# Kernel optimization log

Measured on AMD Instinct MI355X. Metric: run time of the kernel, lower is better.

The kernel has to match this reference:

```python
import jax, jax.numpy as jnp
import numpy as np

B, S, C = 16, 2048, 512
E = S            # embed_dim == seq_len (RMSNorm applied on transposed seq axis)
H = 4 * E        # FFN hidden
LAMBDA_INIT = float(0.8 - 0.6 * np.exp(-0.3 * 1.0))  # layer_index = 1
SCALE = E ** (-0.25)
K = 5            # decomposition moving-average kernel


def rmsnorm(x, w, eps=1e-8):
    return x * jax.lax.rsqrt(jnp.mean(x * x, axis=-1, keepdims=True) + eps) * w


def decompose(a):
    # DLinear-style series decomposition: replicate-padded moving average along seq
    pad = (K - 1) // 2
    ap = jnp.concatenate([jnp.repeat(a[:, :1], pad, axis=1), a, jnp.repeat(a[:, -1:], pad, axis=1)], axis=1)
    n = a.shape[1]
    trend = sum(ap[:, i:i + n] for i in range(K)) / K
    return trend, a - trend


def setup_inputs() -> dict:
    key = jax.random.key(0)
    ks = jax.random.split(key, 12)
    p = lambda i, shape, s=0.02: jax.random.normal(ks[i], shape, jnp.float32) * s
    return {
        "x": jax.random.normal(ks[0], (B, S, C), jnp.float32),
        "ln_attn_w": jnp.ones((E,), jnp.float32),
        "q12_w": p(1, (E, 2 * E)), "q12_b": jnp.zeros((2 * E,), jnp.float32),
        "k12_w": p(2, (E, 2 * E)), "k12_b": jnp.zeros((2 * E,), jnp.float32),
        "v_w": p(3, (E, E)), "v_b": jnp.zeros((E,), jnp.float32),
        "lambda_q1": p(4, (E,), 0.1), "lambda_k1": p(5, (E,), 0.1),
        "lambda_q2": p(6, (E,), 0.1), "lambda_k2": p(7, (E,), 0.1),
        "norm_w": jnp.ones((E,), jnp.float32),
        "ln_ff_w": jnp.ones((E,), jnp.float32),
        "ff_w1": p(8, (E, H)), "ff_b1": jnp.zeros((H,), jnp.float32),
        "ff_w2": p(9, (H, E)), "ff_b2": jnp.zeros((E,), jnp.float32),
    }


def reference(x, ln_attn_w, q12_w, q12_b, k12_w, k12_b, v_w, v_b,
              lambda_q1, lambda_k1, lambda_q2, lambda_k2,
              norm_w, ln_ff_w, ff_w1, ff_b1, ff_w2, ff_b2):
    # pre-attention RMSNorm over the seq axis (via transpose)
    a = jnp.swapaxes(rmsnorm(jnp.swapaxes(x, -1, -2), ln_attn_w), -1, -2)  # [B,S,C]
    trend, seasonal = decompose(a)
    # project seq dim of trend/seasonal (iTransformer style: channels are tokens)
    q = jnp.swapaxes(trend, -1, -2) @ q12_w + q12_b      # [B,C,2S]
    q1, q2 = jnp.split(q, 2, axis=-1)                    # [B,C,S] each
    k = jnp.swapaxes(seasonal, -1, -2) @ k12_w + k12_b   # [B,C,2S]
    k1, k2 = jnp.split(k, 2, axis=-1)                    # [B,C,S]
    v = jnp.swapaxes(a, -1, -2) @ v_w + v_b              # [B,C,S]
    a1 = jnp.einsum('bis,bjs->bij', q1, k1) * SCALE      # [B,C,C]
    a2 = jnp.einsum('bis,bjs->bij', q2, k2) * SCALE      # [B,C,C]
    lam = jnp.exp(jnp.sum(lambda_q1 * lambda_k1)) - jnp.exp(jnp.sum(lambda_q2 * lambda_k2)) + LAMBDA_INIT
    d = jax.nn.softmax(a1, axis=-1) - lam * jax.nn.softmax(a2, axis=-1)
    attn = rmsnorm(d @ v, norm_w) * (1.0 - LAMBDA_INIT)  # [B,C,S]
    x = x + jnp.swapaxes(attn, -1, -2)
    # FFN over the seq axis
    h = rmsnorm(jnp.swapaxes(x, -1, -2), ln_ff_w)        # [B,C,S]
    ff = jax.nn.gelu(h @ ff_w1 + ff_b1, approximate=False) @ ff_w2 + ff_b2
    return x + jnp.swapaxes(ff, -1, -2)
```

## Files before the change

kernel.cpp:

```cpp
#include <hip/hip_runtime.h>
#include <hip/hip_bf16.h>

#define B_ 16
#define S_ 2048
#define C_ 512
#define H_ 8192

#define LAMBDA_INIT_F 0.3555090675909693f
#define ONE_M_LI_F    0.6444909324090307f
#define SCALE_F       0.14865088937534013f

using bf16x8 = __attribute__((ext_vector_type(8))) short;
using f32x4  = __attribute__((ext_vector_type(4))) float;

__device__ __forceinline__ float b2f(ushort u) {
  union { unsigned u; float f; } x; x.u = ((unsigned)u) << 16; return x.f;
}
__device__ __forceinline__ ushort f2b(float f) {
  union { float f; unsigned u; } x; x.f = f;
  unsigned r = x.u + 0x7fffu + ((x.u >> 16) & 1u);
  return (ushort)(r >> 16);
}

__device__ __forceinline__ void load_lds16(const void* g, void* s) {
  __builtin_amdgcn_global_load_lds((const __attribute__((address_space(1))) void*)g,
                                   (__attribute__((address_space(3))) void*)s,
                                   16, 0, 0);
}

#define WAITV4() do { asm volatile("s_waitcnt vmcnt(4)" ::: "memory"); __builtin_amdgcn_sched_barrier(0); } while (0)
#define WAITV0() do { asm volatile("s_waitcnt vmcnt(0)" ::: "memory"); __builtin_amdgcn_sched_barrier(0); } while (0)
#define WAITL0() do { asm volatile("s_waitcnt lgkmcnt(0)" ::: "memory"); __builtin_amdgcn_sched_barrier(0); } while (0)
#define BAR()    __builtin_amdgcn_s_barrier()

template <int EPI>
__global__ __launch_bounds__(512, 1) void gemm256(
    const ushort* __restrict__ A, const ushort* __restrict__ Bt,
    ushort* __restrict__ C, const float* __restrict__ bias,
    const ushort* __restrict__ addm,
    int K, int lda, int ldb, int ldc)
{
  __shared__ ushort lds[65536];
  const int t = threadIdx.x, w = t >> 6, lane = t & 63;
  const int fr = lane & 15, khl = lane >> 4;
  const int wr = w >> 2, wc = w & 3;

  const int gx = gridDim.x;
  const int id = blockIdx.y * gx + blockIdx.x;
  const int nwg = gx * gridDim.y;
  const int swz = (id & 7) * (nwg >> 3) + (id >> 3);
  const int m0 = (swz % gx) * 256, n0 = (swz / gx) * 256;

  const int sl    = (t & 7) ^ ((t >> 3) & 7);
  const int rbase = ((t >> 3) << 1) + (sl >> 2);
  const int khs   = sl & 3;
  const size_t aoff = (size_t)(m0 + rbase) * lda + khs * 8;
  const size_t boff = (size_t)(n0 + rbase) * ldb + khs * 8;
  const size_t jstA = (size_t)128 * lda, jstB = (size_t)128 * ldb;

  int ao[8], bo[4];
#pragma unroll
  for (int m = 0; m < 8; ++m) {
    const int row = wr * 128 + m * 16 + fr, dr = row >> 1;
    const int so = (((row & 1) << 2) + khl) ^ (dr & 7);
    ao[m] = dr * 64 + so * 8;
  }
#pragma unroll
  for (int n = 0; n < 4; ++n) {
    const int row = wc * 64 + n * 16 + fr, dr = row >> 1;
    const int so = (((row & 1) << 2) + khl) ^ (dr & 7);
    bo[n] = 16384 + dr * 64 + so * 8;
  }

  f32x4 acc[8][4] = {};
  const int NT = K >> 6;

#define STAGE_A(ch, nb, k1) do { const ushort* s_ = A + aoff + (k1) + (ch) * 32; \
    ushort* d_ = &lds[(nb) + (ch) * 8192 + w * 512]; \
    load_lds16(s_, d_); load_lds16(s_ + jstA, d_ + 4096); } while (0)
#define STAGE_B(ch, nb, k1) do { const ushort* s_ = Bt + boff + (k1) + (ch) * 32; \
    ushort* d_ = &lds[(nb) + 16384 + (ch) * 8192 + w * 512]; \
    load_lds16(s_, d_); load_lds16(s_ + jstB, d_ + 4096); } while (0)
#define LDA(cb, ch, m) (*(const bf16x8*)&lds[(cb) + (ch) * 8192 + ao[m]])
#define LDB(cb, ch, n) (*(const bf16x8*)&lds[(cb) + (ch) * 8192 + bo[n]])
#define MFMA8(mlo, nf, bg) _Pragma("unroll") for (int m_ = 0; m_ < 8; ++m_) \
    acc[m_][nf] = __builtin_amdgcn_mfma_f32_16x16x32_bf16(af[m_], bg, acc[m_][nf], 0, 0, 0)

  STAGE_A(0, 0, 0); STAGE_B(0, 0, 0); STAGE_A(1, 0, 0); STAGE_B(1, 0, 0);
  WAITV4(); BAR();

  bf16x8 af[8];
  for (int kt = 0; kt < NT - 1; ++kt) {
    const int cb = (kt & 1) << 15, nb = cb ^ 32768;
    const int k1 = (kt + 1) << 6;
    bf16x8 b0, b1;
#pragma unroll
    for (int m = 0; m < 8; ++m) af[m] = LDA(cb, 0, m);
    b0 = LDB(cb, 0, 0); b1 = LDB(cb, 0, 1);
    STAGE_A(0, nb, k1);
    BAR(); WAITL0();
    __builtin_amdgcn_s_setprio(1); MFMA8(0, 0, b0); MFMA8(0, 1, b1); __builtin_amdgcn_s_setprio(0);
    BAR();
    b0 = LDB(cb, 0, 2); b1 = LDB(cb, 0, 3);
    STAGE_B(0, nb, k1);
    WAITV4(); BAR(); WAITL0();
    __builtin_amdgcn_s_setprio(1); MFMA8(0, 2, b0); MFMA8(0, 3, b1); __builtin_amdgcn_s_setprio(0);
    BAR();
#pragma unroll
    for (int m = 0; m < 8; ++m) af[m] = LDA(cb, 1, m);
    b0 = LDB(cb, 1, 0); b1 = LDB(cb, 1, 1);
    STAGE_A(1, nb, k1);
    BAR(); WAITL0();
    __builtin_amdgcn_s_setprio(1); MFMA8(1, 0, b0); MFMA8(1, 1, b1); __builtin_amdgcn_s_setprio(0);
    BAR();
    b0 = LDB(cb, 1, 2); b1 = LDB(cb, 1, 3);
    STAGE_B(1, nb, k1);
    WAITV4(); BAR(); WAITL0();
    __builtin_amdgcn_s_setprio(1); MFMA8(1, 2, b0); MFMA8(1, 3, b1); __builtin_amdgcn_s_setprio(0);
    BAR();
  }
  {
    const int cb = ((NT - 1) & 1) << 15;
    bf16x8 b0, b1;
#pragma unroll
    for (int m = 0; m < 8; ++m) af[m] = LDA(cb, 0, m);
    b0 = LDB(cb, 0, 0); b1 = LDB(cb, 0, 1);
    BAR(); WAITL0();
    MFMA8(0, 0, b0); MFMA8(0, 1, b1);
    BAR();
    b0 = LDB(cb, 0, 2); b1 = LDB(cb, 0, 3);
    WAITV0(); BAR(); WAITL0();
    MFMA8(0, 2, b0); MFMA8(0, 3, b1);
    BAR();
#pragma unroll
    for (int m = 0; m < 8; ++m) af[m] = LDA(cb, 1, m);
    b0 = LDB(cb, 1, 0); b1 = LDB(cb, 1, 1);
    BAR(); WAITL0();
    MFMA8(1, 0, b0); MFMA8(1, 1, b1);
    BAR();
    b0 = LDB(cb, 1, 2); b1 = LDB(cb, 1, 3);
    BAR(); WAITL0();
    MFMA8(1, 2, b0); MFMA8(1, 3, b1);
  }
#undef STAGE_A
#undef STAGE_B
#undef LDA
#undef LDB
#undef MFMA8

  const int r0 = khl * 4;
#pragma unroll
  for (int m = 0; m < 8; ++m)
#pragma unroll
    for (int nf = 0; nf < 4; ++nf) {
      const int gr = m0 + wr * 128 + m * 16 + r0;
      const int gc = n0 + wc * 64 + nf * 16 + fr;
      const float bb = (EPI == 3) ? 0.f : bias[gc];
#pragma unroll
      for (int r = 0; r < 4; ++r) {
        const size_t idx = (size_t)(gr + r) * ldc + gc;
        float v = acc[m][nf][r];
        if constexpr (EPI == 1) v += bb;
        if constexpr (EPI == 2) { v += bb; v = 0.5f * v * (1.f + erff(v * 0.7071067811865475f)); }
        if constexpr (EPI == 4) v += bb + b2f(addm[idx]) + b2f(C[idx]);
        C[idx] = f2b(v);
      }
    }
}

template <int EPI>
__global__ __launch_bounds__(256, 2) void gemm_nt(
    const ushort* __restrict__ Aall, const ushort* __restrict__ Ball,
    void* __restrict__ Call, int K, int lda, int ldb, int ldc,
    long sA, long sB, long sC, long sA2, long sB2, float alpha)
{
  __shared__ ushort lA[4096];
  __shared__ ushort lB[4096];
  const int t = threadIdx.x;
  const int m0 = blockIdx.x * 128, n0 = blockIdx.y * 128;
  const int zb = blockIdx.z & 15, zh = blockIdx.z >> 4;
  const ushort* A  = Aall + (size_t)zb * sA + (size_t)zh * sA2;
  const ushort* Bt = Ball + (size_t)zb * sB + (size_t)zh * sB2;
  const int lane = t & 63;
  const int wave = t >> 6;
  const int wm = (wave >> 1) * 64, wn = (wave & 1) * 64;
  const int fr = lane & 15, kh = lane >> 4;
  f32x4 acc[4][4] = {};
  const int srow = t >> 2;
  const int scol = (t & 3) * 8;
  const size_t ar0 = (size_t)(m0 + srow) * lda + scol;
  const size_t ar1 = (size_t)(m0 + 64 + srow) * lda + scol;
  const size_t br0 = (size_t)(n0 + srow) * ldb + scol;
  const size_t br1 = (size_t)(n0 + 64 + srow) * ldb + scol;
  const int wbase = wave * 512;

  for (int k0 = 0; k0 < K; k0 += 32) {
    __syncthreads();
    load_lds16(A + ar0 + k0,  &lA[wbase]);
    load_lds16(A + ar1 + k0,  &lA[2048 + wbase]);
    load_lds16(Bt + br0 + k0, &lB[wbase]);
    load_lds16(Bt + br1 + k0, &lB[2048 + wbase]);
    __syncthreads();
    bf16x8 af[4], bg[4];
#pragma unroll
    for (int i = 0; i < 4; ++i)
      af[i] = *(const bf16x8*)&lA[(wm + i * 16 + fr) * 32 + kh * 8];
#pragma unroll
    for (int j = 0; j < 4; ++j)
      bg[j] = *(const bf16x8*)&lB[(wn + j * 16 + fr) * 32 + kh * 8];
#pragma unroll
    for (int i = 0; i < 4; ++i)
#pragma unroll
      for (int j = 0; j < 4; ++j)
        acc[i][j] = __builtin_amdgcn_mfma_f32_16x16x32_bf16(af[i], bg[j], acc[i][j], 0, 0, 0);
  }

  const int r0 = kh * 4;
  if constexpr (EPI == 0) {
    float* C = (float*)Call + (size_t)blockIdx.z * sC;
#pragma unroll
    for (int i = 0; i < 4; ++i)
#pragma unroll
      for (int j = 0; j < 4; ++j) {
        const int gr = m0 + wm + i * 16 + r0;
        const int gc = n0 + wn + j * 16 + fr;
#pragma unroll
        for (int r = 0; r < 4; ++r)
          C[(size_t)(gr + r) * ldc + gc] = acc[i][j][r] * alpha;
      }
  } else {
    ushort* C = (ushort*)Call + (size_t)blockIdx.z * sC;
#pragma unroll
    for (int i = 0; i < 4; ++i)
#pragma unroll
      for (int j = 0; j < 4; ++j) {
        const int gr = m0 + wm + i * 16 + r0;
        const int gc = n0 + wn + j * 16 + fr;
#pragma unroll
        for (int r = 0; r < 4; ++r)
          C[(size_t)(gr + r) * ldc + gc] = f2b(acc[i][j][r] * alpha);
      }
  }
}

__device__ __forceinline__ float block_sum(float v, float* red) {
#pragma unroll
  for (int o = 32; o > 0; o >>= 1) v += __shfl_down(v, o, 64);
  __syncthreads();
  if ((threadIdx.x & 63) == 0) red[threadIdx.x >> 6] = v;
  __syncthreads();
  return red[0] + red[1] + red[2] + red[3];
}
__device__ __forceinline__ float block_max(float v, float* red) {
#pragma unroll
  for (int o = 32; o > 0; o >>= 1) v = fmaxf(v, __shfl_down(v, o, 64));
  __syncthreads();
  if ((threadIdx.x & 63) == 0) red[threadIdx.x >> 6] = v;
  __syncthreads();
  return fmaxf(fmaxf(red[0], red[1]), fmaxf(red[2], red[3]));
}

__global__ __launch_bounds__(256) void k_rms_part(const float* __restrict__ x, float* __restrict__ part) {
  const int c = blockIdx.x * 256 + threadIdx.x;
  const int sl = blockIdx.y;
  const int b = blockIdx.z;
  const float* p = x + (size_t)b * S_ * C_ + c;
  const int s0 = sl * 256;
  float s = 0.f;
  for (int i = 0; i < 256; ++i) { float v = p[(size_t)(s0 + i) * C_]; s += v * v; }
  part[((size_t)b * C_ + c) * 8 + sl] = s;
}
__global__ __launch_bounds__(256) void k_rms_fin(const float* __restrict__ part, float* __restrict__ rms1) {
  const int i = blockIdx.x * 256 + threadIdx.x;
  const float* p = part + (size_t)i * 8;
  float s = 0.f;
#pragma unroll
  for (int j = 0; j < 8; ++j) s += p[j];
  rms1[i] = rsqrtf(s * (1.f / S_) + 1e-8f);
}

__global__ __launch_bounds__(256) void k_trans_norm(const float* __restrict__ x, const float* __restrict__ rms1,
                                                    const float* __restrict__ w,
                                                    ushort* __restrict__ aT, ushort* __restrict__ xT) {
  __shared__ float tile[32][33];
  const int s0 = blockIdx.x * 32, c0 = blockIdx.y * 32, b = blockIdx.z;
  const int tx = threadIdx.x, ty = threadIdx.y;
  const float* xb = x + (size_t)b * S_ * C_;
#pragma unroll
  for (int r = 0; r < 4; ++r) {
    const int s = ty + 8 * r;
    tile[s][tx] = xb[(size_t)(s0 + s) * C_ + c0 + tx];
  }
  __syncthreads();
#pragma unroll
  for (int r = 0; r < 4; ++r) {
    const int c = ty + 8 * r;
    const float v = tile[tx][c];
    const float rm = rms1[b * C_ + c0 + c];
    const size_t o = ((size_t)b * C_ + c0 + c) * S_ + s0 + tx;
    xT[o] = f2b(v);
    aT[o] = f2b(v * rm * w[s0 + tx]);
  }
}

__global__ __launch_bounds__(256) void k_wtrans(const float* __restrict__ W, ushort* __restrict__ WT,
                                                int Kd, int Ndstride, int n_base) {
  __shared__ float tile[32][33];
  const int k0 = blockIdx.x * 32, n0 = blockIdx.y * 32;
  const int tx = threadIdx.x, ty = threadIdx.y;
#pragma unroll
  for (int r = 0; r < 4; ++r) {
    const int k = ty + 8 * r;
    tile[k][tx] = W[(size_t)(k0 + k) * Ndstride + n_base + n0 + tx];
  }
  __syncthreads();
#pragma unroll
  for (int r = 0; r < 4; ++r) {
    const int n = ty + 8 * r;
    WT[(size_t)(n0 + n) * Kd + k0 + tx] = f2b(tile[tx][n]);
  }
}

__global__ __launch_bounds__(256) void k_bt(const ushort* __restrict__ in, ushort* __restrict__ out, int R, int CL) {
  __shared__ ushort tile[32][33];
  const int r0 = blockIdx.x * 32, c0 = blockIdx.y * 32;
  const size_t zb = (size_t)blockIdx.z * R * CL;
  const int tx = threadIdx.x, ty = threadIdx.y;
#pragma unroll
  for (int r = 0; r < 4; ++r) {
    const int rr = ty + 8 * r;
    tile[rr][tx] = in[zb + (size_t)(r0 + rr) * CL + c0 + tx];
  }
  __syncthreads();
#pragma unroll
  for (int r = 0; r < 4; ++r) {
    const int cc = ty + 8 * r;
    out[zb + (size_t)(c0 + cc) * R + r0 + tx] = tile[tx][cc];
  }
}

__device__ __forceinline__ float trend5(const ushort* p, int s) {
  float sum = 0.f;
#pragma unroll
  for (int d = -2; d <= 2; ++d) {
    int ss = s + d; ss = ss < 0 ? 0 : (ss > S_ - 1 ? S_ - 1 : ss);
    sum += b2f(p[ss]);
  }
  return sum * 0.2f;
}
__global__ __launch_bounds__(256) void k_dtrend(const ushort* __restrict__ aT, ushort* __restrict__ trT) {
  const size_t i = (size_t)blockIdx.x * 256 + threadIdx.x;
  const int s = (int)(i & (S_ - 1));
  trT[i] = f2b(trend5(aT + (i - s), s));
}
__global__ __launch_bounds__(256) void k_dseason(const ushort* __restrict__ aT, ushort* __restrict__ seT) {
  const size_t i = (size_t)blockIdx.x * 256 + threadIdx.x;
  const int s = (int)(i & (S_ - 1));
  const ushort* p = aT + (i - s);
  seT[i] = f2b(b2f(p[s]) - trend5(p, s));
}

__global__ __launch_bounds__(256) void k_lambda(const float* __restrict__ lq1, const float* __restrict__ lk1,
                                                const float* __restrict__ lq2, const float* __restrict__ lk2,
                                                float* __restrict__ lam) {
  __shared__ float r1[4], r2[4];
  const int t = threadIdx.x;
  float s1 = 0.f, s2 = 0.f;
  for (int i = t; i < S_; i += 256) { s1 += lq1[i] * lk1[i]; s2 += lq2[i] * lk2[i]; }
#pragma unroll
  for (int o = 32; o > 0; o >>= 1) { s1 += __shfl_down(s1, o, 64); s2 += __shfl_down(s2, o, 64); }
  if ((t & 63) == 0) { r1[t >> 6] = s1; r2[t >> 6] = s2; }
  __syncthreads();
  if (t == 0) {
    const float a = r1[0] + r1[1] + r1[2] + r1[3];
    const float b = r2[0] + r2[1] + r2[2] + r2[3];
    *lam = expf(a) - expf(b) + LAMBDA_INIT_F;
  }
}

__global__ __launch_bounds__(256) void k_softmax(const float* __restrict__ a1, const float* __restrict__ a2,
                                                 const float* __restrict__ lamp, ushort* __restrict__ dm) {
  __shared__ float red[4];
  const size_t row = blockIdx.x;
  const float* p1 = a1 + row * 512;
  const float* p2 = a2 + row * 512;
  const int t = threadIdx.x;
  const float v1a = p1[t], v1b = p1[t + 256];
  const float v2a = p2[t], v2b = p2[t + 256];
  const float m1 = block_max(fmaxf(v1a, v1b), red);
  const float m2 = block_max(fmaxf(v2a, v2b), red);
  const float e1a = expf(v1a - m1), e1b = expf(v1b - m1);
  const float e2a = expf(v2a - m2), e2b = expf(v2b - m2);
  const float s1 = block_sum(e1a + e1b, red);
  const float s2 = block_sum(e2a + e2b, red);
  const float i1 = 1.f / s1, i2 = (*lamp) / s2;
  ushort* o = dm + row * 512;
  o[t]       = f2b(e1a * i1 - e2a * i2);
  o[t + 256] = f2b(e1b * i1 - e2b * i2);
}

__global__ __launch_bounds__(256) void k_postattn(const ushort* __restrict__ P, const ushort* __restrict__ xT,
                                                  const float* __restrict__ norm_w, const float* __restrict__ ln_ff_w,
                                                  ushort* __restrict__ attn, ushort* __restrict__ h) {
  __shared__ float red[4];
  const size_t row = blockIdx.x;
  const ushort* p = P + row * S_;
  const int t = threadIdx.x;
  float v[8]; float ss = 0.f;
#pragma unroll
  for (int i = 0; i < 8; ++i) { v[i] = b2f(p[t + 256 * i]); ss += v[i] * v[i]; }
  ss = block_sum(ss, red);
  const float inv = rsqrtf(ss * (1.f / S_) + 1e-8f);
  const ushort* xr = xT + row * S_;
  ushort* ar = attn + row * S_;
  float x2[8]; float ss2 = 0.f;
#pragma unroll
  for (int i = 0; i < 8; ++i) {
    const int s = t + 256 * i;
    const float at = v[i] * inv * norm_w[s] * ONE_M_LI_F;
    ar[s] = f2b(at);
    const float xx = b2f(xr[s]) + at;
    x2[i] = xx; ss2 += xx * xx;
  }
  ss2 = block_sum(ss2, red);
  const float inv2 = rsqrtf(ss2 * (1.f / S_) + 1e-8f);
  ushort* hr = h + row * S_;
#pragma unroll
  for (int i = 0; i < 8; ++i) { const int s = t + 256 * i; hr[s] = f2b(x2[i] * inv2 * ln_ff_w[s]); }
}

__global__ __launch_bounds__(256) void k_final2(const float* __restrict__ x, const ushort* __restrict__ sumT,
                                                float* __restrict__ out) {
  __shared__ float tile[32][33];
  const int s0 = blockIdx.x * 32, c0 = blockIdx.y * 32, b = blockIdx.z;
  const int tx = threadIdx.x, ty = threadIdx.y;
#pragma unroll
  for (int r = 0; r < 4; ++r) {
    const int c = ty + 8 * r;
    tile[c][tx] = b2f(sumT[((size_t)b * C_ + c0 + c) * S_ + s0 + tx]);
  }
  __syncthreads();
#pragma unroll
  for (int r = 0; r < 4; ++r) {
    const int s = ty + 8 * r;
    const size_t o = ((size_t)b * S_ + s0 + s) * C_ + c0 + tx;
    out[o] = x[o] + tile[tx][s];
  }
}

__global__ void k_probe(float* out, float v) { out[0] = v; }

extern "C" void kernel_launch(void* const* d_in, const int* in_sizes, int n_in,
                              void* d_out, int out_size, void* d_ws, size_t ws_size,
                              hipStream_t stream) {
  const float* x       = (const float*)d_in[0];
  const float* ln_attn = (const float*)d_in[1];
  const float* q12_w   = (const float*)d_in[2];
  const float* q12_b   = (const float*)d_in[3];
  const float* k12_w   = (const float*)d_in[4];
  const float* k12_b   = (const float*)d_in[5];
  const float* v_w     = (const float*)d_in[6];
  const float* v_b     = (const float*)d_in[7];
  const float* lq1     = (const float*)d_in[8];
  const float* lk1     = (const float*)d_in[9];
  const float* lq2     = (const float*)d_in[10];
  const float* lk2     = (const float*)d_in[11];
  const float* norm_w  = (const float*)d_in[12];
  const float* ln_ff   = (const float*)d_in[13];
  const float* ff_w1   = (const float*)d_in[14];
  const float* ff_b1   = (const float*)d_in[15];
  const float* ff_w2   = (const float*)d_in[16];
  const float* ff_b2   = (const float*)d_in[17];
  float* out = (float*)d_out;

  if (ws_size < 184844544ull) {
    k_probe<<<1, 1, 0, stream>>>(out, (float)(ws_size >> 20));
    return;
  }

  char* ws = (char*)d_ws;
  ushort* slotA = (ushort*)(ws + 0);
  ushort* slotB = (ushort*)(ws + 33554432);
  ushort* slotC = (ushort*)(ws + 67108864);
  ushort* slotD = (ushort*)(ws + 100663296);
  ushort* slotE = (ushort*)(ws + 134217728);
  ushort* slotF = (ushort*)(ws + 167772160);
  float*  part  = (float*) (ws + 184549376);
  float*  rms1  = (float*) (ws + 184811520);
  float*  lamp  = (float*) (ws + 184844288);

  ushort* aT   = slotA;
  ushort* xT   = slotE;
  ushort* Vm   = slotB;
  ushort* VT   = slotD;
  ushort* trT  = slotB;
  ushort* seT  = slotC;
  ushort* K12  = slotA;
  float*  scr  = (float*)slotC;
  ushort* Pm   = slotB;
  ushort* attn = slotC;
  ushort* hbuf = slotA;
  ushort* ff1T = slotB;
  ushort* ff2T = slotD;
  ushort* ffo  = slotE;
  ushort* wsl  = slotF;
  ushort* dmat = slotF;
  ushort* Qm   = (ushort*)d_out;
  ushort* H1   = (ushort*)d_out;

  const dim3 blk256(256), blk512(512), blkT(32, 8);

  k_rms_part<<<dim3(2, 8, B_), blk256, 0, stream>>>(x, part);
  k_rms_fin<<<dim3(32), blk256, 0, stream>>>(part, rms1);
  k_trans_norm<<<dim3(64, 16, B_), blkT, 0, stream>>>(x, rms1, ln_attn, aT, xT);

  k_wtrans<<<dim3(64, 64), blkT, 0, stream>>>(v_w, wsl, 2048, 2048, 0);
  gemm256<1><<<dim3(32, 8), blk512, 0, stream>>>(aT, wsl, Vm, v_b, nullptr, 2048, 2048, 2048, 2048);
  k_bt<<<dim3(16, 64, B_), blkT, 0, stream>>>(Vm, VT, 512, 2048);

  k_dtrend<<<dim3(65536), blk256, 0, stream>>>(aT, trT);
  k_wtrans<<<dim3(64, 128), blkT, 0, stream>>>(q12_w, wsl, 2048, 4096, 0);
  gemm256<1><<<dim3(32, 16), blk512, 0, stream>>>(trT, wsl, Qm, q12_b, nullptr, 2048, 2048, 2048, 4096);

  k_dseason<<<dim3(65536), blk256, 0, stream>>>(aT, seT);
  k_lambda<<<dim3(1), blk256, 0, stream>>>(lq1, lk1, lq2, lk2, lamp);
  k_wtrans<<<dim3(64, 128), blkT, 0, stream>>>(k12_w, wsl, 2048, 4096, 0);
  gemm256<1><<<dim3(32, 16), blk512, 0, stream>>>(seT, wsl, K12, k12_b, nullptr, 2048, 2048, 2048, 4096);

  gemm_nt<0><<<dim3(4, 4, 32), blk256, 0, stream>>>(Qm, K12, scr, 2048, 4096, 4096, 512,
                                                    512L * 4096, 512L * 4096, 512L * 512,
                                                    2048L, 2048L, SCALE_F);

  k_softmax<<<dim3(8192), blk256, 0, stream>>>(scr, scr + 4194304, lamp, dmat);
  gemm_nt<3><<<dim3(4, 16, B_), blk256, 0, stream>>>(dmat, VT, Pm, 512, 512, 512, 2048,
                                                     512L * 512, 2048L * 512, 512L * 2048,
                                                     0, 0, 1.f);

  k_postattn<<<dim3(8192), blk256, 0, stream>>>(Pm, xT, norm_w, ln_ff, attn, hbuf);

  k_wtrans<<<dim3(64, 256), blkT, 0, stream>>>(ff_w1, ff1T, 2048, 8192, 0);
  k_wtrans<<<dim3(256, 64), blkT, 0, stream>>>(ff_w2, ff2T, 8192, 2048, 0);

  gemm256<2><<<dim3(32, 16), blk512, 0, stream>>>(hbuf, ff1T, H1, ff_b1, nullptr,
                                                  2048, 2048, 2048, 4096);
  gemm256<3><<<dim3(32, 8), blk512, 0, stream>>>(H1, ff2T, ffo, nullptr, nullptr,
                                                 4096, 4096, 8192, 2048);
  gemm256<2><<<dim3(32, 16), blk512, 0, stream>>>(hbuf, ff1T + (size_t)4096 * 2048, H1,
                                                  ff_b1 + 4096, nullptr, 2048, 2048, 2048, 4096);
  gemm256<4><<<dim3(32, 8), blk512, 0, stream>>>(H1, ff2T + 4096, ffo, ff_b2, attn,
                                                 4096, 4096, 8192, 2048);

  k_final2<<<dim3(64, 16, B_), blkT, 0, stream>>>(x, ffo, out);
}
```

Before: 1.329 ms.

## Restructure GEMM LDS pipeline into four 32-wide K stages with deeper prefetch

Measured after the change: 1.346 ms. No clear change (+1.3%).

```diff
diff --git a/kernel.cpp b/kernel.cpp
--- a/kernel.cpp
+++ b/kernel.cpp
@@ -28,6 +28,7 @@
                                    16, 0, 0);
 }
 
+#define WAITV8() do { asm volatile("s_waitcnt vmcnt(8)" ::: "memory"); __builtin_amdgcn_sched_barrier(0); } while (0)
 #define WAITV4() do { asm volatile("s_waitcnt vmcnt(4)" ::: "memory"); __builtin_amdgcn_sched_barrier(0); } while (0)
 #define WAITV0() do { asm volatile("s_waitcnt vmcnt(0)" ::: "memory"); __builtin_amdgcn_sched_barrier(0); } while (0)
 #define WAITL0() do { asm volatile("s_waitcnt lgkmcnt(0)" ::: "memory"); __builtin_amdgcn_sched_barrier(0); } while (0)
@@ -51,101 +52,111 @@
   const int swz = (id & 7) * (nwg >> 3) + (id >> 3);
   const int m0 = (swz % gx) * 256, n0 = (swz / gx) * 256;
 
-  const int sl    = (t & 7) ^ ((t >> 3) & 7);
-  const int rbase = ((t >> 3) << 1) + (sl >> 2);
-  const int khs   = sl & 3;
-  const size_t aoff = (size_t)(m0 + rbase) * lda + khs * 8;
-  const size_t boff = (size_t)(n0 + rbase) * ldb + khs * 8;
+  const int rs = t >> 2;
+  const int cs = (t & 3) ^ (rs & 3);
+  const size_t aoff = (size_t)(m0 + rs) * lda + cs * 8;
+  const size_t boff = (size_t)(n0 + rs) * ldb + cs * 8;
   const size_t jstA = (size_t)128 * lda, jstB = (size_t)128 * ldb;
 
   int ao[8], bo[4];
 #pragma unroll
   for (int m = 0; m < 8; ++m) {
-    const int row = wr * 128 + m * 16 + fr, dr = row >> 1;
-    const int so = (((row & 1) << 2) + khl) ^ (dr & 7);
-    ao[m] = dr * 64 + so * 8;
+    const int row = wr * 128 + m * 16 + fr;
+    ao[m] = row * 32 + ((khl ^ (row & 3)) * 8);
   }
 #pragma unroll
   for (int n = 0; n < 4; ++n) {
-    const int row = wc * 64 + n * 16 + fr, dr = row >> 1;
-    const int so = (((row & 1) << 2) + khl) ^ (dr & 7);
-    bo[n] = 16384 + dr * 64 + so * 8;
+    const int row = wc * 64 + n * 16 + fr;
+    bo[n] = 8192 + row * 32 + ((khl ^ (row & 3)) * 8);
   }
 
   f32x4 acc[8][4] = {};
   const int NT = K >> 6;
 
-#define STAGE_A(ch, nb, k1) do { const ushort* s_ = A + aoff + (k1) + (ch) * 32; \
-    ushort* d_ = &lds[(nb) + (ch) * 8192 + w * 512]; \
+#define STAGE_A(u) do { const ushort* s_ = A + aoff + (size_t)(u) * 32; \
+    ushort* d_ = &lds[((u) & 3) * 16384 + w * 512]; \
     load_lds16(s_, d_); load_lds16(s_ + jstA, d_ + 4096); } while (0)
-#define STAGE_B(ch, nb, k1) do { const ushort* s_ = Bt + boff + (k1) + (ch) * 32; \
-    ushort* d_ = &lds[(nb) + 16384 + (ch) * 8192 + w * 512]; \
+#define STAGE_B(u) do { const ushort* s_ = Bt + boff + (size_t)(u) * 32; \
+    ushort* d_ = &lds[((u) & 3) * 16384 + 8192 + w * 512]; \
     load_lds16(s_, d_); load_lds16(s_ + jstB, d_ + 4096); } while (0)
-#define LDA(cb, ch, m) (*(const bf16x8*)&lds[(cb) + (ch) * 8192 + ao[m]])
-#define LDB(cb, ch, n) (*(const bf16x8*)&lds[(cb) + (ch) * 8192 + bo[n]])
-#define MFMA8(mlo, nf, bg) _Pragma("unroll") for (int m_ = 0; m_ < 8; ++m_) \
+#define LDA8(u) _Pragma("unroll") for (int m_ = 0; m_ < 8; ++m_) \
+    af[m_] = *(const bf16x8*)&lds[((u) & 3) * 16384 + ao[m_]]
+#define LDB1(u, n) (*(const bf16x8*)&lds[((u) & 3) * 16384 + bo[n]])
+#define MFMA8(nf, bg) _Pragma("unroll") for (int m_ = 0; m_ < 8; ++m_) \
     acc[m_][nf] = __builtin_amdgcn_mfma_f32_16x16x32_bf16(af[m_], bg, acc[m_][nf], 0, 0, 0)
-
-  STAGE_A(0, 0, 0); STAGE_B(0, 0, 0); STAGE_A(1, 0, 0); STAGE_B(1, 0, 0);
-  WAITV4(); BAR();
-
-  bf16x8 af[8];
-  for (int kt = 0; kt < NT - 1; ++kt) {
-    const int cb = (kt & 1) << 15, nb = cb ^ 32768;
-    const int k1 = (kt + 1) << 6;
-    bf16x8 b0, b1;
-#pragma unroll
-    for (int m = 0; m < 8; ++m) af[m] = LDA(cb, 0, m);
-    b0 = LDB(cb, 0, 0); b1 = LDB(cb, 0, 1);
-    STAGE_A(0, nb, k1);
-    BAR(); WAITL0();
-    __builtin_amdgcn_s_setprio(1); MFMA8(0, 0, b0); MFMA8(0, 1, b1); __builtin_amdgcn_s_setprio(0);
+#define PRIO1() __builtin_amdgcn_s_setprio(1)
+#define PRIO0() __builtin_amdgcn_s_setprio(0)
+
+  STAGE_A(0); STAGE_B(0); STAGE_A(1); STAGE_B(1); STAGE_A(2); STAGE_B(2);
+  WAITV8(); BAR();
+
+  bf16x8 af[8], b0, b1;
+  for (int kt = 0; kt < NT - 2; ++kt) {
+    const int u0 = 2 * kt, u1 = u0 + 1;
+    LDA8(u0); b0 = LDB1(u0, 0); b1 = LDB1(u0, 1);
+    STAGE_A(u0 + 3);
+    BAR(); WAITL0();
+    PRIO1(); MFMA8(0, b0); MFMA8(1, b1); PRIO0();
     BAR();
-    b0 = LDB(cb, 0, 2); b1 = LDB(cb, 0, 3);
-    STAGE_B(0, nb, k1);
-    WAITV4(); BAR(); WAITL0();
-    __builtin_amdgcn_s_setprio(1); MFMA8(0, 2, b0); MFMA8(0, 3, b1); __builtin_amdgcn_s_setprio(0);
+    b0 = LDB1(u0, 2); b1 = LDB1(u0, 3);
+    STAGE_B(u0 + 3);
+    BAR(); WAITL0();
+    PRIO1(); MFMA8(2, b0); MFMA8(3, b1); PRIO0();
+    WAITV8(); BAR();
+    LDA8(u1); b0 = LDB1(u1, 0); b1 = LDB1(u1, 1);
+    STAGE_A(u0 + 4);
+    BAR(); WAITL0();
+    PRIO1(); MFMA8(0, b0); MFMA8(1, b1); PRIO0();
     BAR();
-#pragma unroll
-    for (int m = 0; m < 8; ++m) af[m] = LDA(cb, 1, m);
-    b0 = LDB(cb, 1, 0); b1 = LDB(cb, 1, 1);
-    STAGE_A(1, nb, k1);
-    BAR(); WAITL0();
-    __builtin_amdgcn_s_setprio(1); MFMA8(1, 0, b0); MFMA8(1, 1, b1); __builtin_amdgcn_s_setprio(0);
+    b0 = LDB1(u1, 2); b1 = LDB1(u1, 3);
+    STAGE_B(u0 + 4);
+    BAR(); WAITL0();
+    PRIO1(); MFMA8(2, b0); MFMA8(3, b1); PRIO0();
+    WAITV8(); BAR();
+  }
+  {
+    const int u0 = 2 * (NT - 2), u1 = u0 + 1;
+    LDA8(u0); b0 = LDB1(u0, 0); b1 = LDB1(u0, 1);
+    STAGE_A(u0 + 3);
+    BAR(); WAITL0();
+    PRIO1(); MFMA8(0, b0); MFMA8(1, b1); PRIO0();
     BAR();
-    b0 = LDB(cb, 1, 2); b1 = LDB(cb, 1, 3);
-    STAGE_B(1, nb, k1);
-    WAITV4(); BAR(); WAITL0();
-    __builtin_amdgcn_s_setprio(1); MFMA8(1, 2, b0); MFMA8(1, 3, b1); __builtin_amdgcn_s_setprio(0);
+    b0 = LDB1(u0, 2); b1 = LDB1(u0, 3);
+    STAGE_B(u0 + 3);
+    BAR(); WAITL0();
+    PRIO1(); MFMA8(2, b0); MFMA8(3, b1); PRIO0();
+    WAITV8(); BAR();
+    LDA8(u1); b0 = LDB1(u1, 0); b1 = LDB1(u1, 1);
+    BAR(); WAITL0();
+    PRIO1(); MFMA8(0, b0); MFMA8(1, b1); PRIO0();
     BAR();
+    b0 = LDB1(u1, 2); b1 = LDB1(u1, 3);
+    BAR(); WAITL0();
+    PRIO1(); MFMA8(2, b0); MFMA8(3, b1); PRIO0();
+    WAITV4(); BAR();
   }
   {
-    const int cb = ((NT - 1) & 1) << 15;
-    bf16x8 b0, b1;
-#pragma unroll
-    for (int m = 0; m < 8; ++m) af[m] = LDA(cb, 0, m);
-    b0 = LDB(cb, 0, 0); b1 = LDB(cb, 0, 1);
-    BAR(); WAITL0();
-    MFMA8(0, 0, b0); MFMA8(0, 1, b1);
+    const int u0 = 2 * (NT - 1), u1 = u0 + 1;
+    LDA8(u0); b0 = LDB1(u0, 0); b1 = LDB1(u0, 1);
+    BAR(); WAITL0();
+    PRIO1(); MFMA8(0, b0); MFMA8(1, b1); PRIO0();
     BAR();
-    b0 = LDB(cb, 0, 2); b1 = LDB(cb, 0, 3);
-    WAITV0(); BAR(); WAITL0();
-    MFMA8(0, 2, b0); MFMA8(0, 3, b1);
+    b0 = LDB1(u0, 2); b1 = LDB1(u0, 3);
+    BAR(); WAITL0();
+    PRIO1(); MFMA8(2, b0); MFMA8(3, b1); PRIO0();
+    WAITV0(); BAR();
+    LDA8(u1); b0 = LDB1(u1, 0); b1 = LDB1(u1, 1);
+    BAR(); WAITL0();
+    PRIO1(); MFMA8(0, b0); MFMA8(1, b1); PRIO0();
     BAR();
-#pragma unroll
-    for (int m = 0; m < 8; ++m) af[m] = LDA(cb, 1, m);
-    b0 = LDB(cb, 1, 0); b1 = LDB(cb, 1, 1);
-    BAR(); WAITL0();
-    MFMA8(1, 0, b0); MFMA8(1, 1, b1);
-    BAR();
-    b0 = LDB(cb, 1, 2); b1 = LDB(cb, 1, 3);
-    BAR(); WAITL0();
-    MFMA8(1, 2, b0); MFMA8(1, 3, b1);
+    b0 = LDB1(u1, 2); b1 = LDB1(u1, 3);
+    WAITL0();
+    MFMA8(2, b0); MFMA8(3, b1);
   }
 #undef STAGE_A
 #undef STAGE_B
-#undef LDA
-#undef LDB
+#undef LDA8
+#undef LDB1
 #undef MFMA8
 
   const int r0 = khl * 4;
```

## Restructure GEMM main loop into four-stage k32 LDS ring pipeline

Applied to the files above, without the earlier changes.

New measurement: 1.297 ms. -2.4%, faster.

```diff
diff --git a/kernel.cpp b/kernel.cpp
--- a/kernel.cpp
+++ b/kernel.cpp
@@ -28,8 +28,9 @@
                                    16, 0, 0);
 }
 
-#define WAITV4() do { asm volatile("s_waitcnt vmcnt(4)" ::: "memory"); __builtin_amdgcn_sched_barrier(0); } while (0)
-#define WAITV0() do { asm volatile("s_waitcnt vmcnt(0)" ::: "memory"); __builtin_amdgcn_sched_barrier(0); } while (0)
+#define WAITV8() asm volatile("s_waitcnt vmcnt(8)" ::: "memory")
+#define WAITV4() asm volatile("s_waitcnt vmcnt(4)" ::: "memory")
+#define WAITV0() asm volatile("s_waitcnt vmcnt(0)" ::: "memory")
 #define WAITL0() do { asm volatile("s_waitcnt lgkmcnt(0)" ::: "memory"); __builtin_amdgcn_sched_barrier(0); } while (0)
 #define BAR()    __builtin_amdgcn_s_barrier()
 
@@ -69,84 +70,62 @@
   for (int n = 0; n < 4; ++n) {
     const int row = wc * 64 + n * 16 + fr, dr = row >> 1;
     const int so = (((row & 1) << 2) + khl) ^ (dr & 7);
-    bo[n] = 16384 + dr * 64 + so * 8;
+    bo[n] = 8192 + dr * 64 + so * 8;
   }
 
   f32x4 acc[8][4] = {};
-  const int NT = K >> 6;
-
-#define STAGE_A(ch, nb, k1) do { const ushort* s_ = A + aoff + (k1) + (ch) * 32; \
-    ushort* d_ = &lds[(nb) + (ch) * 8192 + w * 512]; \
-    load_lds16(s_, d_); load_lds16(s_ + jstA, d_ + 4096); } while (0)
-#define STAGE_B(ch, nb, k1) do { const ushort* s_ = Bt + boff + (k1) + (ch) * 32; \
-    ushort* d_ = &lds[(nb) + 16384 + (ch) * 8192 + w * 512]; \
-    load_lds16(s_, d_); load_lds16(s_ + jstB, d_ + 4096); } while (0)
-#define LDA(cb, ch, m) (*(const bf16x8*)&lds[(cb) + (ch) * 8192 + ao[m]])
-#define LDB(cb, ch, n) (*(const bf16x8*)&lds[(cb) + (ch) * 8192 + bo[n]])
-#define MFMA8(mlo, nf, bg) _Pragma("unroll") for (int m_ = 0; m_ < 8; ++m_) \
-    acc[m_][nf] = __builtin_amdgcn_mfma_f32_16x16x32_bf16(af[m_], bg, acc[m_][nf], 0, 0, 0)
-
-  STAGE_A(0, 0, 0); STAGE_B(0, 0, 0); STAGE_A(1, 0, 0); STAGE_B(1, 0, 0);
-  WAITV4(); BAR();
-
-  bf16x8 af[8];
-  for (int kt = 0; kt < NT - 1; ++kt) {
-    const int cb = (kt & 1) << 15, nb = cb ^ 32768;
-    const int k1 = (kt + 1) << 6;
-    bf16x8 b0, b1;
-#pragma unroll
-    for (int m = 0; m < 8; ++m) af[m] = LDA(cb, 0, m);
-    b0 = LDB(cb, 0, 0); b1 = LDB(cb, 0, 1);
-    STAGE_A(0, nb, k1);
-    BAR(); WAITL0();
-    __builtin_amdgcn_s_setprio(1); MFMA8(0, 0, b0); MFMA8(0, 1, b1); __builtin_amdgcn_s_setprio(0);
+  const int U = K >> 5;
+
+#define STAGE_U(u) do { \
+    const ushort* sa_ = A  + aoff + (size_t)(u) * 32; \
+    const ushort* sb_ = Bt + boff + (size_t)(u) * 32; \
+    ushort* da_ = &lds[((u) & 3) * 16384 + w * 512]; \
+    load_lds16(sa_, da_); load_lds16(sa_ + jstA, da_ + 4096); \
+    load_lds16(sb_, da_ + 8192); load_lds16(sb_ + jstB, da_ + 12288); } while (0)
+#define LDFRAG(u) do { const int sb_ = ((u) & 3) * 16384; \
+    _Pragma("unroll") for (int m_ = 0; m_ < 8; ++m_) af[m_] = *(const bf16x8*)&lds[sb_ + ao[m_]]; \
+    _Pragma("unroll") for (int n_ = 0; n_ < 4; ++n_) bg[n_] = *(const bf16x8*)&lds[sb_ + bo[n_]]; } while (0)
+#define MFMA32() do { __builtin_amdgcn_s_setprio(1); \
+    _Pragma("unroll") for (int m_ = 0; m_ < 8; ++m_) \
+    _Pragma("unroll") for (int n_ = 0; n_ < 4; ++n_) \
+      acc[m_][n_] = __builtin_amdgcn_mfma_f32_16x16x32_bf16(af[m_], bg[n_], acc[m_][n_], 0, 0, 0); \
+    __builtin_amdgcn_s_setprio(0); } while (0)
+
+  STAGE_U(0); STAGE_U(1); STAGE_U(2);
+  WAITV8(); BAR();
+
+  bf16x8 af[8], bg[4];
+#pragma unroll 4
+  for (int u = 0; u <= U - 4; ++u) {
+    LDFRAG(u);
+    STAGE_U(u + 3);
+    WAITL0();
+    MFMA32();
+    WAITV8();
     BAR();
-    b0 = LDB(cb, 0, 2); b1 = LDB(cb, 0, 3);
-    STAGE_B(0, nb, k1);
-    WAITV4(); BAR(); WAITL0();
-    __builtin_amdgcn_s_setprio(1); MFMA8(0, 2, b0); MFMA8(0, 3, b1); __builtin_amdgcn_s_setprio(0);
+  }
+  {
+    LDFRAG(U - 3);
+    WAITL0();
+    MFMA32();
+    WAITV4();
     BAR();
-#pragma unroll
-    for (int m = 0; m < 8; ++m) af[m] = LDA(cb, 1, m);
-    b0 = LDB(cb, 1, 0); b1 = LDB(cb, 1, 1);
-    STAGE_A(1, nb, k1);
-    BAR(); WAITL0();
-    __builtin_amdgcn_s_setprio(1); MFMA8(1, 0, b0); MFMA8(1, 1, b1); __builtin_amdgcn_s_setprio(0);
+  }
+  {
+    LDFRAG(U - 2);
+    WAITL0();
+    MFMA32();
+    WAITV0();
     BAR();
-    b0 = LDB(cb, 1, 2); b1 = LDB(cb, 1, 3);
-    STAGE_B(1, nb, k1);
-    WAITV4(); BAR(); WAITL0();
-    __builtin_amdgcn_s_setprio(1); MFMA8(1, 2, b0); MFMA8(1, 3, b1); __builtin_amdgcn_s_setprio(0);
-    BAR();
   }
   {
-    const int cb = ((NT - 1) & 1) << 15;
-    bf16x8 b0, b1;
-#pragma unroll
-    for (int m = 0; m < 8; ++m) af[m] = LDA(cb, 0, m);
-    b0 = LDB(cb, 0, 0); b1 = LDB(cb, 0, 1);
-    BAR(); WAITL0();
-    MFMA8(0, 0, b0); MFMA8(0, 1, b1);
-    BAR();
-    b0 = LDB(cb, 0, 2); b1 = LDB(cb, 0, 3);
-    WAITV0(); BAR(); WAITL0();
-    MFMA8(0, 2, b0); MFMA8(0, 3, b1);
-    BAR();
-#pragma unroll
-    for (int m = 0; m < 8; ++m) af[m] = LDA(cb, 1, m);
-    b0 = LDB(cb, 1, 0); b1 = LDB(cb, 1, 1);
-    BAR(); WAITL0();
-    MFMA8(1, 0, b0); MFMA8(1, 1, b1);
-    BAR();
-    b0 = LDB(cb, 1, 2); b1 = LDB(cb, 1, 3);
-    BAR(); WAITL0();
-    MFMA8(1, 2, b0); MFMA8(1, 3, b1);
-  }
-#undef STAGE_A
-#undef STAGE_B
-#undef LDA
-#undef LDB
-#undef MFMA8
+    LDFRAG(U - 1);
+    WAITL0();
+    MFMA32();
+  }
+#undef STAGE_U
+#undef LDFRAG
+#undef MFMA32
 
   const int r0 = khl * 4;
 #pragma unroll
```
